# Kernel tuning notes

Measured on AMD Instinct MI355X. Metric: run time of the kernel, lower is better.

Reference implementation:

```python
import jax, jax.numpy as jnp
import numpy as np
from jax import lax

ITERS = 16
ALPHA = 0.3
SMOOTH = 1.0


def _maxpool3d(x, win):
    dims = (1, 1) + win
    return lax.reduce_window(x, -jnp.inf, lax.max, dims, (1,) * 5, 'SAME')


def soft_erode(x):
    # min-pool along each axis separately (clDice 3D soft erosion)
    e1 = -_maxpool3d(-x, (3, 1, 1))
    e2 = -_maxpool3d(-x, (1, 3, 1))
    e3 = -_maxpool3d(-x, (1, 1, 3))
    return jnp.minimum(jnp.minimum(e1, e2), e3)


def soft_dilate(x):
    return _maxpool3d(x, (3, 3, 3))


def soft_open(x):
    return soft_dilate(soft_erode(x))


def soft_skel(x, n_iter):
    skel = jax.nn.relu(x - soft_open(x))

    def body(carry, _):
        img, skel = carry
        img = soft_erode(img)
        delta = jax.nn.relu(img - soft_open(img))
        skel = skel + jax.nn.relu(delta - skel * delta)
        return (img, skel), None

    (_, skel), _ = lax.scan(body, (x, skel), None, length=n_iter)
    return skel


def soft_dice(y_true, y_pred, smooth):
    intersection = jnp.sum(y_true * y_pred)
    coeff = (2.0 * intersection + smooth) / (jnp.sum(y_true) + jnp.sum(y_pred) + smooth)
    return 1.0 - coeff


def setup_inputs() -> dict:
    key = jax.random.key(0)
    k1, k2 = jax.random.split(key)
    shape = (4, 1, 128, 128, 128)
    y_pred = jax.random.normal(k1, shape, dtype=jnp.float32)  # logits
    # binary ground-truth mask as float32
    y_true = jnp.round(jax.random.uniform(k2, shape, dtype=jnp.float32))
    return {"y_pred": y_pred, "y_true": y_true}


def reference(y_pred, y_true):
    yp = jax.nn.sigmoid(y_pred)
    dice = soft_dice(y_true, yp, SMOOTH)
    skel_pred = soft_skel(yp, ITERS)
    skel_true = soft_skel(y_true, ITERS)
    tprec = (jnp.sum(skel_pred * y_true) + SMOOTH) / (jnp.sum(skel_pred) + SMOOTH)
    tsens = (jnp.sum(skel_true * yp) + SMOOTH) / (jnp.sum(skel_true) + SMOOTH)
    cl_dice = 1.0 - 2.0 * (tprec * tsens) / (tprec + tsens)
    return (1.0 - ALPHA) * dice + ALPHA * cl_dice
```

## Files before the change

kernel.cpp:

```cpp
#include <hip/hip_runtime.h>
#include <cmath>

#define NB 4
#define ND 128
#define NH 128
#define NW 128
#define NVOL_VOX (ND * NH * NW)
#define NVOX (NB * NVOL_VOX)

#define THREADS 256
#define TX 32
#define TY 16
#define SSTR 13
#define RSTR 9
#define ZS4 ((NH * NW) >> 2)

__device__ __forceinline__ float4 f4min(float4 a, float4 b) {
    return make_float4(fminf(a.x, b.x), fminf(a.y, b.y), fminf(a.z, b.z), fminf(a.w, b.w));
}
__device__ __forceinline__ float4 f4max(float4 a, float4 b) {
    return make_float4(fmaxf(a.x, b.x), fmaxf(a.y, b.y), fmaxf(a.z, b.z), fmaxf(a.w, b.w));
}
__device__ __forceinline__ float4 f4relu_sub(float4 a, float4 b) {
    return make_float4(fmaxf(a.x - b.x, 0.f), fmaxf(a.y - b.y, 0.f),
                       fmaxf(a.z - b.z, 0.f), fmaxf(a.w - b.w, 0.f));
}
__device__ __forceinline__ float4 f4winmin(float4 lf, float4 cc, float4 rt) {
    float4 o;
    o.x = fminf(fminf(lf.w, cc.x), cc.y);
    o.y = fminf(fminf(cc.x, cc.y), cc.z);
    o.z = fminf(fminf(cc.y, cc.z), cc.w);
    o.w = fminf(fminf(cc.z, cc.w), rt.x);
    return o;
}
__device__ __forceinline__ float4 f4winmax(float4 lf, float4 cc, float4 rt) {
    float4 o;
    o.x = fmaxf(fmaxf(lf.w, cc.x), cc.y);
    o.y = fmaxf(fmaxf(cc.x, cc.y), cc.z);
    o.z = fmaxf(fmaxf(cc.y, cc.z), cc.w);
    o.w = fmaxf(fmaxf(cc.z, cc.w), rt.x);
    return o;
}

__device__ __forceinline__ float block_reduce(float v, float* sbuf) {
    for (int off = 32; off > 0; off >>= 1) v += __shfl_down(v, off, 64);
    int lane = threadIdx.x & 63;
    int wid  = threadIdx.x >> 6;
    if (lane == 0) sbuf[wid] = v;
    __syncthreads();
    float r = 0.f;
    if (wid == 0) {
        r = (lane < (int)(blockDim.x >> 6)) ? sbuf[lane] : 0.f;
        for (int off = 8; off > 0; off >>= 1) r += __shfl_down(r, off, 64);
    }
    __syncthreads();
    return r;
}

#define SIG_BLOCKS 1024
__global__ void sigmoid_reduce_kernel(const float4* __restrict__ logits,
                                      const float4* __restrict__ yt,
                                      float4* __restrict__ yp,
                                      float* __restrict__ part) {
    __shared__ float sbuf[THREADS / 64];
    const int n4 = NVOX / 4;
    float sp = 0.f, st = 0.f, stp = 0.f;
    for (int i = blockIdx.x * blockDim.x + threadIdx.x; i < n4;
         i += gridDim.x * blockDim.x) {
        float4 l = logits[i];
        float4 t = yt[i];
        float4 p;
        p.x = 1.f / (1.f + expf(-l.x));
        p.y = 1.f / (1.f + expf(-l.y));
        p.z = 1.f / (1.f + expf(-l.z));
        p.w = 1.f / (1.f + expf(-l.w));
        yp[i] = p;
        sp  += p.x + p.y + p.z + p.w;
        st  += t.x + t.y + t.z + t.w;
        stp += t.x * p.x + t.y * p.y + t.z * p.z + t.w * p.w;
    }
    float a = block_reduce(sp, sbuf);
    float b = block_reduce(st, sbuf);
    float c = block_reduce(stp, sbuf);
    if (threadIdx.x == 0) {
        part[blockIdx.x]        = a;
        part[1024 + blockIdx.x] = b;
        part[2048 + blockIdx.x] = c;
    }
}

__global__ __launch_bounds__(256, 4)
void init_step_kernel(const float* __restrict__ srcA, const float* __restrict__ srcB,
                      float* __restrict__ skel, int zchunks) {
    __shared__ float4 srcS[2][22 * SSTR];
    __shared__ float4 e1S [2][20 * SSTR];
    __shared__ float4 rxS [2][18 * RSTR];

    const float4 INF4  = make_float4(INFINITY, INFINITY, INFINITY, INFINITY);
    const float4 MINF4 = make_float4(-INFINITY, -INFINITY, -INFINITY, -INFINITY);

    const int zlen  = ND / zchunks;
    const int v     = blockIdx.z / zchunks;
    const int chunk = blockIdx.z - v * zchunks;
    const int z0    = chunk * zlen;
    const int tx0   = blockIdx.x * TX;
    const int ty0   = blockIdx.y * TY;
    const int tid   = threadIdx.x;

    const float* src = srcB ? (v < 4 ? srcA + (size_t)v * NVOL_VOX
                                     : srcB + (size_t)(v - 4) * NVOL_VOX)
                            : srcA + (size_t)v * NVOL_VOX;
    const float4* src4 = (const float4*)src;
    float4* skl4 = (float4*)(skel + (size_t)v * NVOL_VOX);

    const int fy = tid / 10, qx = tid - (tid / 10) * 10;
    const bool tOK = tid < 220;
    const bool aE1 = tOK && fy >= 1 && fy < 21;
    const bool aRx = tOK && fy >= 2 && fy < 20 && qx >= 1 && qx < 9;
    const bool aC  = tOK && fy >= 3 && fy < 19 && qx >= 1 && qx < 9;
    const int gy = ty0 + fy - 3;
    const int gx4 = tx0 + (qx - 1) * 4;
    const bool gOK = tOK && (unsigned)gy < NH && (unsigned)gx4 < NW;
    const int colBase = gOK ? ((gy * NW + gx4) >> 2) : 0;
    const int iSrc = fy * SSTR + qx + 1;
    const int iE1  = (fy - 1) * SSTR + qx + 1;
    const int iRx  = (fy - 2) * RSTR + (qx - 1);

    for (int l = tid; l < 2 * 22 * 2; l += THREADS)
        srcS[l & 1][(l >> 2) * SSTR + ((l >> 1) & 1) * 11] = INF4;
    for (int l = tid; l < 2 * 20 * 2; l += THREADS)
        e1S[l & 1][(l >> 2) * SSTR + ((l >> 1) & 1) * 11] = INF4;
    __syncthreads();

    float4 srcF[6], e1F[2], rxF[2], mxyF[3];
#pragma unroll
    for (int i = 0; i < 6; ++i) srcF[i] = INF4;
    e1F[0] = e1F[1] = INF4;
    rxF[0] = rxF[1] = MINF4;
    mxyF[0] = mxyF[1] = mxyF[2] = MINF4;

    const int NSTEP = zlen + 8;
    for (int sb = 0; sb < NSTEP; sb += 6) {
#pragma unroll
        for (int u = 0; u < 6; ++u) {
            const int zL = z0 - 3 + (sb + u);
            const int sl  = u & 1;
            const int slp = sl ^ 1;

            {
                float4 vv = INF4;
                if ((unsigned)zL < ND && zL < z0 + zlen + 3 && gOK)
                    vv = src4[zL * ZS4 + colBase];
                srcF[u % 6] = vv;
                if (tOK) srcS[sl][iSrc] = vv;
            }
            {
                const int z = zL - 1;
                float4 vv = INF4;
                if (aE1 && (unsigned)z < ND) {
                    const float4* S = srcS[slp];
                    float4 xm = f4winmin(S[iSrc - 1], srcF[(u + 5) % 6], S[iSrc + 1]);
                    vv = f4min(f4min(xm, S[iSrc - SSTR]),
                               f4min(S[iSrc + SSTR],
                                     f4min(srcF[(u + 4) % 6], srcF[u % 6])));
                }
                e1F[u % 2] = vv;
                if (aE1) e1S[sl][iE1] = vv;
            }
            {
                float4 rxv = MINF4;
                if (aRx) {
                    const float4* S = e1S[slp];
                    rxv = f4winmax(S[iE1 - 1], e1F[(u + 1) % 2], S[iE1 + 1]);
                    rxS[sl][iRx] = rxv;
                }
                float4 m = MINF4;
                if (aC)
                    m = f4max(f4max(rxF[(u + 1) % 2], rxS[slp][iRx - RSTR]),
                              rxS[slp][iRx + RSTR]);
                rxF[u % 2] = rxv;
                mxyF[u % 3] = m;
            }
            {
                const int z = zL - 4;
                if (aC && z >= z0 && z < z0 + zlen) {
                    float4 dil = f4max(f4max(mxyF[0], mxyF[1]), mxyF[2]);
                    skl4[z * ZS4 + colBase] = f4relu_sub(srcF[(u + 2) % 6], dil);
                }
            }
            __syncthreads();
        }
    }
}

template <int RED>
__global__ __launch_bounds__(256, 2)
void skel_pair_kernel(const float* __restrict__ srcA, const float* __restrict__ srcB,
                      float* __restrict__ imgOut, float* __restrict__ skel,
                      int zchunks,
                      const float* __restrict__ othA, const float* __restrict__ othB,
                      float* __restrict__ part, int offBase) {
    __shared__ float4 srcS[2][24 * SSTR];
    __shared__ float4 e1S [2][22 * SSTR];
    __shared__ float4 e2S [2][20 * SSTR];
    __shared__ float4 e3S [2][18 * SSTR];
    __shared__ float4 rxAS[2][18 * RSTR];
    __shared__ float4 rxBS[2][18 * RSTR];

    const float4 INF4  = make_float4(INFINITY, INFINITY, INFINITY, INFINITY);
    const float4 MINF4 = make_float4(-INFINITY, -INFINITY, -INFINITY, -INFINITY);
    const float4 ZERO4 = make_float4(0.f, 0.f, 0.f, 0.f);

    const int zlen  = ND / zchunks;
    const int v     = blockIdx.z / zchunks;
    const int chunk = blockIdx.z - v * zchunks;
    const int z0    = chunk * zlen;
    const int tx0   = blockIdx.x * TX;
    const int ty0   = blockIdx.y * TY;
    const int tid   = threadIdx.x;

    const float* src = srcB ? (v < 4 ? srcA + (size_t)v * NVOL_VOX
                                     : srcB + (size_t)(v - 4) * NVOL_VOX)
                            : srcA + (size_t)v * NVOL_VOX;
    const float4* src4 = (const float4*)src;
    float4* img4 = imgOut ? (float4*)(imgOut + (size_t)v * NVOL_VOX) : nullptr;
    float4* skl4 = (float4*)(skel + (size_t)v * NVOL_VOX);
    const float4* oth4 = nullptr;
    if (RED) {
        const float* oth = othB ? (v < 4 ? othA + (size_t)v * NVOL_VOX
                                         : othB + (size_t)(v - 4) * NVOL_VOX)
                                : othA + (size_t)v * NVOL_VOX;
        oth4 = (const float4*)oth;
    }

    const int fy = tid / 10, qx = tid - (tid / 10) * 10;
    const bool tOK = tid < 240;
    const bool aE1 = tOK && fy >= 1 && fy < 23;
    const bool aE2 = tOK && fy >= 2 && fy < 22;
    const bool aE3 = tOK && fy >= 3 && fy < 21;
    const bool aRx = aE3 && qx >= 1 && qx < 9;
    const bool aC  = tOK && fy >= 4 && fy < 20 && qx >= 1 && qx < 9;
    const int gy = ty0 + fy - 4;
    const int gx4 = tx0 + (qx - 1) * 4;
    const bool gOK = tOK && (unsigned)gy < NH && (unsigned)gx4 < NW;
    const int colBase = gOK ? ((gy * NW + gx4) >> 2) : 0;
    const int iSrc = fy * SSTR + qx + 1;
    const int iE1  = (fy - 1) * SSTR + qx + 1;
    const int iE2  = (fy - 2) * SSTR + qx + 1;
    const int iE3  = (fy - 3) * SSTR + qx + 1;
    const int iRx  = (fy - 3) * RSTR + (qx - 1);

    for (int l = tid; l < 2 * 24 * 2; l += THREADS)
        srcS[l & 1][(l >> 2) * SSTR + ((l >> 1) & 1) * 11] = INF4;
    for (int l = tid; l < 2 * 22 * 2; l += THREADS)
        e1S[l & 1][(l >> 2) * SSTR + ((l >> 1) & 1) * 11] = INF4;
    for (int l = tid; l < 2 * 20 * 2; l += THREADS)
        e2S[l & 1][(l >> 2) * SSTR + ((l >> 1) & 1) * 11] = INF4;
    for (int l = tid; l < 2 * 18 * 2; l += THREADS)
        e3S[l & 1][(l >> 2) * SSTR + ((l >> 1) & 1) * 11] = INF4;
    __syncthreads();

    float4 srcF[3], e1F[6], e2F[6], e3F[2], rxAF[2], rxBF[2], mxyAF[3], mxyBF[3], dAF[2];
    float4 sklF[6], othF[6];
#pragma unroll
    for (int i = 0; i < 3; ++i) srcF[i] = INF4;
#pragma unroll
    for (int i = 0; i < 6; ++i) { e1F[i] = INF4; e2F[i] = INF4; sklF[i] = ZERO4; othF[i] = ZERO4; }
    e3F[0] = e3F[1] = INF4;
    rxAF[0] = rxAF[1] = MINF4;
    rxBF[0] = rxBF[1] = MINF4;
    mxyAF[0] = mxyAF[1] = mxyAF[2] = MINF4;
    mxyBF[0] = mxyBF[1] = mxyBF[2] = MINF4;
    dAF[0] = dAF[1] = ZERO4;

    float accS = 0.f, accSO = 0.f;
    const int NSTEP = zlen + 10;

    for (int sb = 0; sb < NSTEP; sb += 6) {
#pragma unroll
        for (int u = 0; u < 6; ++u) {
            const int zL = z0 - 4 + (sb + u);
            const int sl  = u & 1;
            const int slp = sl ^ 1;

            {
                float4 vv = INF4;
                if ((unsigned)zL < ND && zL < z0 + zlen + 4 && gOK)
                    vv = src4[zL * ZS4 + colBase];
                srcF[u % 3] = vv;
                if (tOK) srcS[sl][iSrc] = vv;
            }
            {
                const int zp = zL - 3;
                const bool pOK = aC && zp >= z0 && zp < z0 + zlen;
                float4 sv = ZERO4;
                if (pOK) sv = skl4[zp * ZS4 + colBase];
                sklF[u] = sv;
                if (RED) {
                    float4 ov = ZERO4;
                    if (pOK) ov = oth4[zp * ZS4 + colBase];
                    othF[u] = ov;
                }
            }
            {
                const int z = zL - 1;
                float4 vv = INF4;
                if (aE1 && (unsigned)z < ND) {
                    const float4* S = srcS[slp];
                    float4 xm = f4winmin(S[iSrc - 1], srcF[(u + 2) % 3], S[iSrc + 1]);
                    vv = f4min(f4min(xm, S[iSrc - SSTR]),
                               f4min(S[iSrc + SSTR],
                                     f4min(srcF[(u + 1) % 3], srcF[u % 3])));
                }
                e1F[u % 6] = vv;
                if (aE1) e1S[sl][iE1] = vv;
            }
            {
                const int z = zL - 2;
                float4 vv = INF4;
                if (aE2) {
                    const float4* S = e1S[slp];
                    float4 xm = f4winmin(S[iE1 - 1], e1F[(u + 5) % 6], S[iE1 + 1]);
                    vv = f4min(f4min(xm, S[iE1 - SSTR]),
                               f4min(S[iE1 + SSTR],
                                     f4min(e1F[(u + 4) % 6], e1F[u % 6])));
                    e2S[sl][iE2] = vv;
                    if (img4 && aC && z >= z0 && z < z0 + zlen)
                        img4[z * ZS4 + colBase] = vv;
                }
                e2F[u % 6] = vv;
            }
            {
                float4 vv = INF4;
                if (aE3) {
                    const float4* S = e2S[slp];
                    float4 xm = f4winmin(S[iE2 - 1], e2F[(u + 5) % 6], S[iE2 + 1]);
                    vv = f4min(f4min(xm, S[iE2 - SSTR]),
                               f4min(S[iE2 + SSTR],
                                     f4min(e2F[(u + 4) % 6], e2F[u % 6])));
                    e3S[sl][iE3] = vv;
                }
                e3F[u % 2] = vv;
            }
            {
                float4 ra = MINF4, rb = MINF4;
                if (aRx) {
                    const float4* SA = e2S[slp];
                    const float4* SB = e3S[slp];
                    ra = f4winmax(SA[iE2 - 1], e2F[(u + 5) % 6], SA[iE2 + 1]);
                    rb = f4winmax(SB[iE3 - 1], e3F[(u + 1) % 2], SB[iE3 + 1]);
                    rxAS[sl][iRx] = ra;
                    rxBS[sl][iRx] = rb;
                }
                float4 mA = MINF4, mB = MINF4;
                if (aC) {
                    mA = f4max(f4max(rxAF[(u + 1) % 2], rxAS[slp][iRx - RSTR]),
                               rxAS[slp][iRx + RSTR]);
                    mB = f4max(f4max(rxBF[(u + 1) % 2], rxBS[slp][iRx - RSTR]),
                               rxBS[slp][iRx + RSTR]);
                }
                rxAF[u % 2] = ra;
                rxBF[u % 2] = rb;
                mxyAF[u % 3] = mA;
                mxyBF[u % 3] = mB;
            }
            {
                float4 dilA = f4max(f4max(mxyAF[0], mxyAF[1]), mxyAF[2]);
                dAF[u % 2] = f4relu_sub(e1F[(u + 2) % 6], dilA);
            }
            {
                const int z = zL - 6;
                if (aC && z >= z0 && z < z0 + zlen) {
                    float4 dilB = f4max(f4max(mxyBF[0], mxyBF[1]), mxyBF[2]);
                    float4 dB = f4relu_sub(e2F[(u + 2) % 6], dilB);
                    float4 da = dAF[(u + 1) % 2];
                    int gi = z * ZS4 + colBase;
                    float4 sv = sklF[(u + 3) % 6];
                    float4 s1, s2;
                    s1.x = sv.x + fmaxf(da.x - sv.x * da.x, 0.f);
                    s1.y = sv.y + fmaxf(da.y - sv.y * da.y, 0.f);
                    s1.z = sv.z + fmaxf(da.z - sv.z * da.z, 0.f);
                    s1.w = sv.w + fmaxf(da.w - sv.w * da.w, 0.f);
                    s2.x = s1.x + fmaxf(dB.x - s1.x * dB.x, 0.f);
                    s2.y = s1.y + fmaxf(dB.y - s1.y * dB.y, 0.f);
                    s2.z = s1.z + fmaxf(dB.z - s1.z * dB.z, 0.f);
                    s2.w = s1.w + fmaxf(dB.w - s1.w * dB.w, 0.f);
                    skl4[gi] = s2;
                    if (RED) {
                        accS += s2.x + s2.y + s2.z + s2.w;
                        float4 o = othF[(u + 3) % 6];
                        accSO += s2.x * o.x + s2.y * o.y + s2.z * o.z + s2.w * o.w;
                    }
                }
            }
            __syncthreads();
        }
    }

    if (RED) {
        float* sbuf = (float*)srcS;
        float r1 = block_reduce(accS, sbuf);
        float r2 = block_reduce(accSO, sbuf);
        if (tid == 0) {
            int halfSel = (othB && v >= 4) ? 1 : 0;
            int A = (offBase + 2 * halfSel) * 1024;
            int zslot = chunk + zchunks * (v & 3);
            int bid = blockIdx.x + 4 * (blockIdx.y + 8 * zslot);
            part[A + bid] = r1;
            part[A + 1024 + bid] = r2;
        }
    }
}

__global__ void finalize_kernel(const float* __restrict__ part, float* __restrict__ out) {
    __shared__ float sbuf[THREADS / 64];
    float s[7];
#pragma unroll
    for (int k = 0; k < 7; ++k) {
        float local = 0.f;
        for (int i = threadIdx.x; i < 1024; i += THREADS) local += part[k * 1024 + i];
        s[k] = block_reduce(local, sbuf);
    }
    if (threadIdx.x == 0) {
        const float smooth = 1.0f;
        const float alpha = 0.3f;
        float dice = 1.f - (2.f * s[2] + smooth) / (s[1] + s[0] + smooth);
        float tprec = (s[4] + smooth) / (s[3] + smooth);
        float tsens = (s[6] + smooth) / (s[5] + smooth);
        float cl = 1.f - 2.f * (tprec * tsens) / (tprec + tsens);
        out[0] = (1.f - alpha) * dice + alpha * cl;
    }
}

extern "C" void kernel_launch(void* const* d_in, const int* in_sizes, int n_in,
                              void* d_out, int out_size, void* d_ws, size_t ws_size,
                              hipStream_t stream) {
    const float* y_pred = (const float*)d_in[0];
    const float* y_true = (const float*)d_in[1];
    float* out = (float*)d_out;

    char* ws = (char*)d_ws;
    float* part = (float*)ws;
    float* yp = (float*)(ws + 32768);
    const size_t NB4 = (size_t)NVOX;
    const size_t need_batched = 32768 + 7 * NB4 * sizeof(float);

    hipMemsetAsync(part, 0, 7 * 1024 * sizeof(float), stream);
    sigmoid_reduce_kernel<<<SIG_BLOCKS, THREADS, 0, stream>>>(
        (const float4*)y_pred, (const float4*)y_true, (float4*)yp, part);

    if (ws_size >= need_batched) {
        float* ping = yp + NB4;
        float* pong = ping + 2 * NB4;
        float* S    = pong + 2 * NB4;
        const int zc = 2;
        dim3 grid(NW / TX, NH / TY, zc * 8);

        init_step_kernel<<<grid, THREADS, 0, stream>>>(yp, y_true, S, zc);

        float* bufs[2] = {ping, pong};
        for (int i = 0; i < 8; ++i) {
            const float* sA = (i == 0) ? yp : bufs[(i + 1) & 1];
            const float* sB = (i == 0) ? y_true : nullptr;
            float* oimg = (i < 7) ? bufs[i & 1] : nullptr;
            if (i < 7)
                skel_pair_kernel<0><<<grid, THREADS, 0, stream>>>(
                    sA, sB, oimg, S, zc, nullptr, nullptr, nullptr, 0);
            else
                skel_pair_kernel<1><<<grid, THREADS, 0, stream>>>(
                    sA, sB, oimg, S, zc, y_true, yp, part, 3);
        }
    } else {
        float* ping = yp + NB4;
        float* pong = ping + NB4;
        float* Sp   = pong + NB4;
        float* St   = Sp + NB4;
        const int zc = 4;
        dim3 grid(NW / TX, NH / TY, zc * 4);

        auto run = [&](const float* x, float* S, const float* other, int offBase) {
            init_step_kernel<<<grid, THREADS, 0, stream>>>(x, nullptr, S, zc);
            float* bufs[2] = {ping, pong};
            for (int i = 0; i < 8; ++i) {
                const float* sA = (i == 0) ? x : bufs[(i + 1) & 1];
                float* oimg = (i < 7) ? bufs[i & 1] : nullptr;
                if (i < 7)
                    skel_pair_kernel<0><<<grid, THREADS, 0, stream>>>(
                        sA, nullptr, oimg, S, zc, nullptr, nullptr, nullptr, 0);
                else
                    skel_pair_kernel<1><<<grid, THREADS, 0, stream>>>(
                        sA, nullptr, oimg, S, zc, other, nullptr, part, offBase);
            }
        };
        run(yp, Sp, y_true, 3);
        run(y_true, St, yp, 5);
    }

    finalize_kernel<<<1, THREADS, 0, stream>>>(part, out);
}
```

Measured before the change: 1.044 ms.

## Fuse initial skeleton step into first paired erosion kernel

Removes the standalone init_step kernel and folds its work into a new INIT variant of skel_pair_kernel. That variant computes the initial relu(x - open(x)) skeleton alongside the first two erosion iterations, which saves one full pass over the source volumes and one skeleton write/read round trip. The x-window min/max helpers now load single scalar neighbours from shared memory instead of whole float4s, cutting LDS traffic. In exchange the INIT path uses more registers and an extra shared buffer, which could lower occupancy.

After: 984.7 us. 1.06x faster.

```diff
diff --git a/kernel.cpp b/kernel.cpp
--- a/kernel.cpp
+++ b/kernel.cpp
@@ -25,20 +25,20 @@
     return make_float4(fmaxf(a.x - b.x, 0.f), fmaxf(a.y - b.y, 0.f),
                        fmaxf(a.z - b.z, 0.f), fmaxf(a.w - b.w, 0.f));
 }
-__device__ __forceinline__ float4 f4winmin(float4 lf, float4 cc, float4 rt) {
+__device__ __forceinline__ float4 f4winmin_s(float lfw, float4 cc, float rtx) {
     float4 o;
-    o.x = fminf(fminf(lf.w, cc.x), cc.y);
+    o.x = fminf(fminf(lfw, cc.x), cc.y);
     o.y = fminf(fminf(cc.x, cc.y), cc.z);
     o.z = fminf(fminf(cc.y, cc.z), cc.w);
-    o.w = fminf(fminf(cc.z, cc.w), rt.x);
+    o.w = fminf(fminf(cc.z, cc.w), rtx);
     return o;
 }
-__device__ __forceinline__ float4 f4winmax(float4 lf, float4 cc, float4 rt) {
+__device__ __forceinline__ float4 f4winmax_s(float lfw, float4 cc, float rtx) {
     float4 o;
-    o.x = fmaxf(fmaxf(lf.w, cc.x), cc.y);
+    o.x = fmaxf(fmaxf(lfw, cc.x), cc.y);
     o.y = fmaxf(fmaxf(cc.x, cc.y), cc.z);
     o.z = fmaxf(fmaxf(cc.y, cc.z), cc.w);
-    o.w = fmaxf(fmaxf(cc.z, cc.w), rt.x);
+    o.w = fmaxf(fmaxf(cc.z, cc.w), rtx);
     return o;
 }
 
@@ -89,111 +89,7 @@
     }
 }
 
-__global__ __launch_bounds__(256, 4)
-void init_step_kernel(const float* __restrict__ srcA, const float* __restrict__ srcB,
-                      float* __restrict__ skel, int zchunks) {
-    __shared__ float4 srcS[2][22 * SSTR];
-    __shared__ float4 e1S [2][20 * SSTR];
-    __shared__ float4 rxS [2][18 * RSTR];
-
-    const float4 INF4  = make_float4(INFINITY, INFINITY, INFINITY, INFINITY);
-    const float4 MINF4 = make_float4(-INFINITY, -INFINITY, -INFINITY, -INFINITY);
-
-    const int zlen  = ND / zchunks;
-    const int v     = blockIdx.z / zchunks;
-    const int chunk = blockIdx.z - v * zchunks;
-    const int z0    = chunk * zlen;
-    const int tx0   = blockIdx.x * TX;
-    const int ty0   = blockIdx.y * TY;
-    const int tid   = threadIdx.x;
-
-    const float* src = srcB ? (v < 4 ? srcA + (size_t)v * NVOL_VOX
-                                     : srcB + (size_t)(v - 4) * NVOL_VOX)
-                            : srcA + (size_t)v * NVOL_VOX;
-    const float4* src4 = (const float4*)src;
-    float4* skl4 = (float4*)(skel + (size_t)v * NVOL_VOX);
-
-    const int fy = tid / 10, qx = tid - (tid / 10) * 10;
-    const bool tOK = tid < 220;
-    const bool aE1 = tOK && fy >= 1 && fy < 21;
-    const bool aRx = tOK && fy >= 2 && fy < 20 && qx >= 1 && qx < 9;
-    const bool aC  = tOK && fy >= 3 && fy < 19 && qx >= 1 && qx < 9;
-    const int gy = ty0 + fy - 3;
-    const int gx4 = tx0 + (qx - 1) * 4;
-    const bool gOK = tOK && (unsigned)gy < NH && (unsigned)gx4 < NW;
-    const int colBase = gOK ? ((gy * NW + gx4) >> 2) : 0;
-    const int iSrc = fy * SSTR + qx + 1;
-    const int iE1  = (fy - 1) * SSTR + qx + 1;
-    const int iRx  = (fy - 2) * RSTR + (qx - 1);
-
-    for (int l = tid; l < 2 * 22 * 2; l += THREADS)
-        srcS[l & 1][(l >> 2) * SSTR + ((l >> 1) & 1) * 11] = INF4;
-    for (int l = tid; l < 2 * 20 * 2; l += THREADS)
-        e1S[l & 1][(l >> 2) * SSTR + ((l >> 1) & 1) * 11] = INF4;
-    __syncthreads();
-
-    float4 srcF[6], e1F[2], rxF[2], mxyF[3];
-#pragma unroll
-    for (int i = 0; i < 6; ++i) srcF[i] = INF4;
-    e1F[0] = e1F[1] = INF4;
-    rxF[0] = rxF[1] = MINF4;
-    mxyF[0] = mxyF[1] = mxyF[2] = MINF4;
-
-    const int NSTEP = zlen + 8;
-    for (int sb = 0; sb < NSTEP; sb += 6) {
-#pragma unroll
-        for (int u = 0; u < 6; ++u) {
-            const int zL = z0 - 3 + (sb + u);
-            const int sl  = u & 1;
-            const int slp = sl ^ 1;
-
-            {
-                float4 vv = INF4;
-                if ((unsigned)zL < ND && zL < z0 + zlen + 3 && gOK)
-                    vv = src4[zL * ZS4 + colBase];
-                srcF[u % 6] = vv;
-                if (tOK) srcS[sl][iSrc] = vv;
-            }
-            {
-                const int z = zL - 1;
-                float4 vv = INF4;
-                if (aE1 && (unsigned)z < ND) {
-                    const float4* S = srcS[slp];
-                    float4 xm = f4winmin(S[iSrc - 1], srcF[(u + 5) % 6], S[iSrc + 1]);
-                    vv = f4min(f4min(xm, S[iSrc - SSTR]),
-                               f4min(S[iSrc + SSTR],
-                                     f4min(srcF[(u + 4) % 6], srcF[u % 6])));
-                }
-                e1F[u % 2] = vv;
-                if (aE1) e1S[sl][iE1] = vv;
-            }
-            {
-                float4 rxv = MINF4;
-                if (aRx) {
-                    const float4* S = e1S[slp];
-                    rxv = f4winmax(S[iE1 - 1], e1F[(u + 1) % 2], S[iE1 + 1]);
-                    rxS[sl][iRx] = rxv;
-                }
-                float4 m = MINF4;
-                if (aC)
-                    m = f4max(f4max(rxF[(u + 1) % 2], rxS[slp][iRx - RSTR]),
-                              rxS[slp][iRx + RSTR]);
-                rxF[u % 2] = rxv;
-                mxyF[u % 3] = m;
-            }
-            {
-                const int z = zL - 4;
-                if (aC && z >= z0 && z < z0 + zlen) {
-                    float4 dil = f4max(f4max(mxyF[0], mxyF[1]), mxyF[2]);
-                    skl4[z * ZS4 + colBase] = f4relu_sub(srcF[(u + 2) % 6], dil);
-                }
-            }
-            __syncthreads();
-        }
-    }
-}
-
-template <int RED>
+template <int RED, int INIT>
 __global__ __launch_bounds__(256, 2)
 void skel_pair_kernel(const float* __restrict__ srcA, const float* __restrict__ srcB,
                       float* __restrict__ imgOut, float* __restrict__ skel,
@@ -206,6 +102,7 @@
     __shared__ float4 e3S [2][18 * SSTR];
     __shared__ float4 rxAS[2][18 * RSTR];
     __shared__ float4 rxBS[2][18 * RSTR];
+    __shared__ float4 rxCS[2][18 * RSTR];
 
     const float4 INF4  = make_float4(INFINITY, INFINITY, INFINITY, INFINITY);
     const float4 MINF4 = make_float4(-INFINITY, -INFINITY, -INFINITY, -INFINITY);
@@ -260,18 +157,23 @@
         e3S[l & 1][(l >> 2) * SSTR + ((l >> 1) & 1) * 11] = INF4;
     __syncthreads();
 
-    float4 srcF[3], e1F[6], e2F[6], e3F[2], rxAF[2], rxBF[2], mxyAF[3], mxyBF[3], dAF[2];
+    constexpr int SD = INIT ? 6 : 3;
+    float4 srcF[SD], e1F[6], e2F[6], e3F[2], rxAF[2], rxBF[2], mxyAF[3], mxyBF[3], dAF[2];
     float4 sklF[6], othF[6];
+    float4 rxCF[2], mxyCF[3], d0F[3];
 #pragma unroll
-    for (int i = 0; i < 3; ++i) srcF[i] = INF4;
+    for (int i = 0; i < SD; ++i) srcF[i] = INF4;
 #pragma unroll
     for (int i = 0; i < 6; ++i) { e1F[i] = INF4; e2F[i] = INF4; sklF[i] = ZERO4; othF[i] = ZERO4; }
     e3F[0] = e3F[1] = INF4;
     rxAF[0] = rxAF[1] = MINF4;
     rxBF[0] = rxBF[1] = MINF4;
+    rxCF[0] = rxCF[1] = MINF4;
     mxyAF[0] = mxyAF[1] = mxyAF[2] = MINF4;
     mxyBF[0] = mxyBF[1] = mxyBF[2] = MINF4;
+    mxyCF[0] = mxyCF[1] = mxyCF[2] = MINF4;
     dAF[0] = dAF[1] = ZERO4;
+    d0F[0] = d0F[1] = d0F[2] = ZERO4;
 
     float accS = 0.f, accSO = 0.f;
     const int NSTEP = zlen + 10;
@@ -287,10 +189,10 @@
                 float4 vv = INF4;
                 if ((unsigned)zL < ND && zL < z0 + zlen + 4 && gOK)
                     vv = src4[zL * ZS4 + colBase];
-                srcF[u % 3] = vv;
+                srcF[u % SD] = vv;
                 if (tOK) srcS[sl][iSrc] = vv;
             }
-            {
+            if (!INIT) {
                 const int zp = zL - 3;
                 const bool pOK = aC && zp >= z0 && zp < z0 + zlen;
                 float4 sv = ZERO4;
@@ -307,10 +209,13 @@
                 float4 vv = INF4;
                 if (aE1 && (unsigned)z < ND) {
                     const float4* S = srcS[slp];
-                    float4 xm = f4winmin(S[iSrc - 1], srcF[(u + 2) % 3], S[iSrc + 1]);
+                    const float* fS = (const float*)S;
+                    float4 cc = INIT ? srcF[(u + 5) % 6] : srcF[(u + 2) % SD];
+                    float4 zm = INIT ? f4min(srcF[(u + 4) % 6], srcF[u % 6])
+                                     : f4min(srcF[(u + 1) % SD], srcF[u % SD]);
+                    float4 xm = f4winmin_s(fS[4 * iSrc - 1], cc, fS[4 * iSrc + 4]);
                     vv = f4min(f4min(xm, S[iSrc - SSTR]),
-                               f4min(S[iSrc + SSTR],
-                                     f4min(srcF[(u + 1) % 3], srcF[u % 3])));
+                               f4min(S[iSrc + SSTR], zm));
                 }
                 e1F[u % 6] = vv;
                 if (aE1) e1S[sl][iE1] = vv;
@@ -320,7 +225,8 @@
                 float4 vv = INF4;
                 if (aE2) {
                     const float4* S = e1S[slp];
-                    float4 xm = f4winmin(S[iE1 - 1], e1F[(u + 5) % 6], S[iE1 + 1]);
+                    const float* fS = (const float*)S;
+                    float4 xm = f4winmin_s(fS[4 * iE1 - 1], e1F[(u + 5) % 6], fS[4 * iE1 + 4]);
                     vv = f4min(f4min(xm, S[iE1 - SSTR]),
                                f4min(S[iE1 + SSTR],
                                      f4min(e1F[(u + 4) % 6], e1F[u % 6])));
@@ -334,7 +240,8 @@
                 float4 vv = INF4;
                 if (aE3) {
                     const float4* S = e2S[slp];
-                    float4 xm = f4winmin(S[iE2 - 1], e2F[(u + 5) % 6], S[iE2 + 1]);
+                    const float* fS = (const float*)S;
+                    float4 xm = f4winmin_s(fS[4 * iE2 - 1], e2F[(u + 5) % 6], fS[4 * iE2 + 4]);
                     vv = f4min(f4min(xm, S[iE2 - SSTR]),
                                f4min(S[iE2 + SSTR],
                                      f4min(e2F[(u + 4) % 6], e2F[u % 6])));
@@ -343,26 +250,39 @@
                 e3F[u % 2] = vv;
             }
             {
-                float4 ra = MINF4, rb = MINF4;
+                float4 ra = MINF4, rb = MINF4, rc = MINF4;
                 if (aRx) {
-                    const float4* SA = e2S[slp];
-                    const float4* SB = e3S[slp];
-                    ra = f4winmax(SA[iE2 - 1], e2F[(u + 5) % 6], SA[iE2 + 1]);
-                    rb = f4winmax(SB[iE3 - 1], e3F[(u + 1) % 2], SB[iE3 + 1]);
+                    const float* fA = (const float*)e2S[slp];
+                    const float* fB = (const float*)e3S[slp];
+                    ra = f4winmax_s(fA[4 * iE2 - 1], e2F[(u + 5) % 6], fA[4 * iE2 + 4]);
+                    rb = f4winmax_s(fB[4 * iE3 - 1], e3F[(u + 1) % 2], fB[4 * iE3 + 4]);
                     rxAS[sl][iRx] = ra;
                     rxBS[sl][iRx] = rb;
-                }
-                float4 mA = MINF4, mB = MINF4;
+                    if (INIT) {
+                        const float* fC = (const float*)e1S[slp];
+                        rc = f4winmax_s(fC[4 * iE1 - 1], e1F[(u + 5) % 6], fC[4 * iE1 + 4]);
+                        rxCS[sl][iRx] = rc;
+                    }
+                }
+                float4 mA = MINF4, mB = MINF4, mC = MINF4;
                 if (aC) {
                     mA = f4max(f4max(rxAF[(u + 1) % 2], rxAS[slp][iRx - RSTR]),
                                rxAS[slp][iRx + RSTR]);
                     mB = f4max(f4max(rxBF[(u + 1) % 2], rxBS[slp][iRx - RSTR]),
                                rxBS[slp][iRx + RSTR]);
+                    if (INIT)
+                        mC = f4max(f4max(rxCF[(u + 1) % 2], rxCS[slp][iRx - RSTR]),
+                                   rxCS[slp][iRx + RSTR]);
                 }
                 rxAF[u % 2] = ra;
                 rxBF[u % 2] = rb;
                 mxyAF[u % 3] = mA;
                 mxyBF[u % 3] = mB;
+                if (INIT) { rxCF[u % 2] = rc; mxyCF[u % 3] = mC; }
+            }
+            if (INIT) {
+                float4 dilC = f4max(f4max(mxyCF[0], mxyCF[1]), mxyCF[2]);
+                d0F[u % 3] = f4relu_sub(srcF[(u + 2) % 6], dilC);
             }
             {
                 float4 dilA = f4max(f4max(mxyAF[0], mxyAF[1]), mxyAF[2]);
@@ -375,7 +295,7 @@
                     float4 dB = f4relu_sub(e2F[(u + 2) % 6], dilB);
                     float4 da = dAF[(u + 1) % 2];
                     int gi = z * ZS4 + colBase;
-                    float4 sv = sklF[(u + 3) % 6];
+                    float4 sv = INIT ? d0F[(u + 1) % 3] : sklF[(u + 3) % 6];
                     float4 s1, s2;
                     s1.x = sv.x + fmaxf(da.x - sv.x * da.x, 0.f);
                     s1.y = sv.y + fmaxf(da.y - sv.y * da.y, 0.f);
@@ -456,19 +376,19 @@
         const int zc = 2;
         dim3 grid(NW / TX, NH / TY, zc * 8);
 
-        init_step_kernel<<<grid, THREADS, 0, stream>>>(yp, y_true, S, zc);
+        skel_pair_kernel<0, 1><<<grid, THREADS, 0, stream>>>(
+            yp, y_true, ping, S, zc, nullptr, nullptr, nullptr, 0);
 
         float* bufs[2] = {ping, pong};
-        for (int i = 0; i < 8; ++i) {
-            const float* sA = (i == 0) ? yp : bufs[(i + 1) & 1];
-            const float* sB = (i == 0) ? y_true : nullptr;
-            float* oimg = (i < 7) ? bufs[i & 1] : nullptr;
-            if (i < 7)
-                skel_pair_kernel<0><<<grid, THREADS, 0, stream>>>(
-                    sA, sB, oimg, S, zc, nullptr, nullptr, nullptr, 0);
+        for (int j = 0; j < 7; ++j) {
+            const float* sA = bufs[j & 1];
+            float* oimg = (j < 6) ? bufs[(j + 1) & 1] : nullptr;
+            if (j < 6)
+                skel_pair_kernel<0, 0><<<grid, THREADS, 0, stream>>>(
+                    sA, nullptr, oimg, S, zc, nullptr, nullptr, nullptr, 0);
             else
-                skel_pair_kernel<1><<<grid, THREADS, 0, stream>>>(
-                    sA, sB, oimg, S, zc, y_true, yp, part, 3);
+                skel_pair_kernel<1, 0><<<grid, THREADS, 0, stream>>>(
+                    sA, nullptr, oimg, S, zc, y_true, yp, part, 3);
         }
     } else {
         float* ping = yp + NB4;
@@ -479,16 +399,17 @@
         dim3 grid(NW / TX, NH / TY, zc * 4);
 
         auto run = [&](const float* x, float* S, const float* other, int offBase) {
-            init_step_kernel<<<grid, THREADS, 0, stream>>>(x, nullptr, S, zc);
+            skel_pair_kernel<0, 1><<<grid, THREADS, 0, stream>>>(
+                x, nullptr, ping, S, zc, nullptr, nullptr, nullptr, 0);
             float* bufs[2] = {ping, pong};
-            for (int i = 0; i < 8; ++i) {
-                const float* sA = (i == 0) ? x : bufs[(i + 1) & 1];
-                float* oimg = (i < 7) ? bufs[i & 1] : nullptr;
-                if (i < 7)
-                    skel_pair_kernel<0><<<grid, THREADS, 0, stream>>>(
+            for (int j = 0; j < 7; ++j) {
+                const float* sA = bufs[j & 1];
+                float* oimg = (j < 6) ? bufs[(j + 1) & 1] : nullptr;
+                if (j < 6)
+                    skel_pair_kernel<0, 0><<<grid, THREADS, 0, stream>>>(
                         sA, nullptr, oimg, S, zc, nullptr, nullptr, nullptr, 0);
                 else
-                    skel_pair_kernel<1><<<grid, THREADS, 0, stream>>>(
+                    skel_pair_kernel<1, 0><<<grid, THREADS, 0, stream>>>(
                         sA, nullptr, oimg, S, zc, other, nullptr, part, offBase);
             }
         };
```
